# Kernel optimization log

Hardware: AMD Instinct MI355X
Metric: run time of the kernel (lower is better)

The kernel has to match this reference:

```python
import jax, jax.numpy as jnp
import numpy as np

IN_F, OUT_F = 512, 512
GRID_SIZE, SPLINE_ORDER = 5, 3
K = GRID_SIZE + SPLINE_ORDER  # 8 basis functions
B, S = 8, 1024


def setup_inputs() -> dict:
    key = jax.random.key(0)
    k1, k2, k3, k4, k5 = jax.random.split(key, 5)
    return {
        "x": jax.random.normal(k1, (B, S, IN_F), dtype=jnp.float32),
        "coeff": jax.random.normal(k2, (OUT_F, IN_F, K), dtype=jnp.float32),
        "scale_base": jax.random.normal(k3, (OUT_F, IN_F), dtype=jnp.float32) * 0.1,
        "scale_spline": jax.random.normal(k4, (OUT_F, IN_F), dtype=jnp.float32),
        "base_bias": jax.random.normal(k5, (OUT_F, IN_F), dtype=jnp.float32),
    }


def reference(x, coeff, scale_base, scale_spline, base_bias):
    batch = x.shape[0]
    in_f = x.shape[-1]
    k = coeff.shape[-1]

    xc = jnp.clip(x.reshape(-1, in_f), -1.0, 1.0)      # (N, in)
    base = jax.nn.silu(xc)                              # (N, in)

    # polynomial basis recurrence: b0 = 1, b1 = x, b_i = 2*x*b_{i-1} - 1
    bases = [jnp.ones_like(xc), xc]
    for _ in range(2, k):
        bases.append(2.0 * xc * bases[-1] - 1.0)
    basis = jnp.stack(bases[:k], axis=-1)               # (N, in, K)

    # spline[n,o] = sum_{i,k} scale_spline[o,i]*coeff[o,i,k]*basis[n,i,k]
    w_spline = scale_spline[..., None] * coeff          # (out, in, K)
    spline_term = jnp.einsum('nik,oik->no', basis, w_spline)
    base_term = base @ scale_base.T                     # (N, out)
    out = base_term + spline_term + jnp.sum(base_bias, axis=1)  # (N, out)

    out = out.reshape(batch, -1, base_bias.shape[0])    # (B, S, out)
    if out.shape[-2] == 1:
        out = out[..., 0, :]
    return out
```

## Files before the change

### kernel.cpp

```cpp
#include <hip/hip_runtime.h>
#include <hip/hip_bf16.h>

#define IN_FEAT 512
#define OUT_FEAT 512
#define NTOK 8192
#define KDIM 4096

#define BM 128
#define BN 64
#define BK 64
#define LDA 72
#define LDB 72

typedef short bf16x8 __attribute__((ext_vector_type(8)));
typedef float f32x4 __attribute__((ext_vector_type(4)));

static __device__ inline short f2bf(float f) {
    union { float f; unsigned u; } v; v.f = f;
    unsigned u = v.u;
    u += 0x7fffu + ((u >> 16) & 1u);
    return (short)(u >> 16);
}

__global__ __launch_bounds__(256) void kan_prep(
    const float* __restrict__ coeff, const float* __restrict__ scale_base,
    const float* __restrict__ scale_spline, const float* __restrict__ base_bias,
    short* __restrict__ Wb, float* __restrict__ bias)
{
    int o = blockIdx.x;
    int tid = threadIdx.x;
    float local = 0.f;
#pragma unroll
    for (int rep = 0; rep < 2; ++rep) {
        int i = tid + rep * 256;
        size_t oi = (size_t)o * IN_FEAT + i;
        const float4* c4 = (const float4*)(coeff + oi * 8);
        float4 ca = c4[0], cb = c4[1];
        float ss = scale_spline[oi];
        float sb = scale_base[oi];
        local += base_bias[oi] + ss * ca.x;
        bf16x8 w;
        w[0] = f2bf(sb);
        w[1] = f2bf(ss * ca.y); w[2] = f2bf(ss * ca.z); w[3] = f2bf(ss * ca.w);
        w[4] = f2bf(ss * cb.x); w[5] = f2bf(ss * cb.y); w[6] = f2bf(ss * cb.z);
        w[7] = f2bf(ss * cb.w);
        *(bf16x8*)(Wb + (size_t)o * KDIM + (size_t)i * 8) = w;
    }
    __shared__ float red[4];
    for (int off = 32; off > 0; off >>= 1) local += __shfl_down(local, off, 64);
    int lane = tid & 63, wv = tid >> 6;
    if (lane == 0) red[wv] = local;
    __syncthreads();
    if (tid == 0) bias[o] = red[0] + red[1] + red[2] + red[3];
}

__global__ __launch_bounds__(256) void kan_gemm(
    const float* __restrict__ x, const short* __restrict__ Wb,
    const float* __restrict__ bias, float* __restrict__ out)
{
    __shared__ __align__(16) short As[BM * LDA];
    __shared__ __align__(16) short Bs[BN * LDB];

    int tid = threadIdx.x;
    int mb = blockIdx.x >> 3;
    int nb = blockIdx.x & 7;
    int m0 = mb * BM, o0 = nb * BN;

    int lane = tid & 63, wv = tid >> 6;
    int wm = wv >> 1, wn = wv & 1;
    int qd = lane >> 4, ln15 = lane & 15;

    f32x4 acc[4][2];
#pragma unroll
    for (int a = 0; a < 4; ++a)
#pragma unroll
        for (int b = 0; b < 2; ++b) acc[a][b] = (f32x4)0.f;

    int n_local = tid >> 1;
    int half = tid & 1;
    const float4* xrow = (const float4*)(x + (size_t)(m0 + n_local) * IN_FEAT);

    for (int it = 0; it < IN_FEAT / 8; ++it) {
        float4 xv = xrow[it * 2 + half];
        float xs[4] = {xv.x, xv.y, xv.z, xv.w};
#pragma unroll
        for (int ii = 0; ii < 4; ++ii) {
            float xc = fminf(fmaxf(xs[ii], -1.f), 1.f);
            float base = xc / (1.f + __expf(-xc));
            bf16x8 fr;
            fr[0] = f2bf(base);
            float t = xc;
            fr[1] = f2bf(t);
#pragma unroll
            for (int f = 2; f < 8; ++f) { t = 2.f * xc * t - 1.f; fr[f] = f2bf(t); }
            *(bf16x8*)&As[n_local * LDA + half * 32 + ii * 8] = fr;
        }
#pragma unroll
        for (int rep = 0; rep < 2; ++rep) {
            int c = tid + rep * 256;
            int row = c >> 3, cc = c & 7;
            bf16x8 wfrag = *(const bf16x8*)(Wb + (size_t)(o0 + row) * KDIM + it * BK + cc * 8);
            *(bf16x8*)&Bs[row * LDB + cc * 8] = wfrag;
        }
        __syncthreads();
#pragma unroll
        for (int kq = 0; kq < 2; ++kq) {
            bf16x8 af[4], bfr[2];
#pragma unroll
            for (int fm = 0; fm < 4; ++fm)
                af[fm] = *(const bf16x8*)&As[(wm * 64 + fm * 16 + ln15) * LDA + kq * 32 + qd * 8];
#pragma unroll
            for (int fn = 0; fn < 2; ++fn)
                bfr[fn] = *(const bf16x8*)&Bs[(wn * 32 + fn * 16 + ln15) * LDB + kq * 32 + qd * 8];
#pragma unroll
            for (int fm = 0; fm < 4; ++fm)
#pragma unroll
                for (int fn = 0; fn < 2; ++fn)
                    acc[fm][fn] = __builtin_amdgcn_mfma_f32_16x16x32_bf16(
                        af[fm], bfr[fn], acc[fm][fn], 0, 0, 0);
        }
        __syncthreads();
    }

#pragma unroll
    for (int fn = 0; fn < 2; ++fn) {
        int o = o0 + wn * 32 + fn * 16 + ln15;
        float bv = bias[o];
#pragma unroll
        for (int fm = 0; fm < 4; ++fm) {
            int r0 = m0 + wm * 64 + fm * 16 + qd * 4;
#pragma unroll
            for (int r = 0; r < 4; ++r)
                out[(size_t)(r0 + r) * OUT_FEAT + o] = acc[fm][fn][r] + bv;
        }
    }
}

extern "C" void kernel_launch(void* const* d_in, const int* in_sizes, int n_in,
                              void* d_out, int out_size, void* d_ws, size_t ws_size,
                              hipStream_t stream) {
    const float* x            = (const float*)d_in[0];
    const float* coeff        = (const float*)d_in[1];
    const float* scale_base   = (const float*)d_in[2];
    const float* scale_spline = (const float*)d_in[3];
    const float* base_bias    = (const float*)d_in[4];
    float* out = (float*)d_out;

    short* Wb   = (short*)d_ws;
    float* bias = (float*)((char*)d_ws + (size_t)OUT_FEAT * KDIM * 2);

    kan_prep<<<OUT_FEAT, 256, 0, stream>>>(coeff, scale_base, scale_spline, base_bias, Wb, bias);
    kan_gemm<<<(NTOK / BM) * (OUT_FEAT / BN), 256, 0, stream>>>(x, Wb, bias, out);
}
```

Before: 156.9 us.

## Materialize bf16 basis matrix and use split-K direct-to-LDS GEMM with atomics

Adds a separate kernel that expands x into the full bf16 basis matrix A (N×4096) in workspace, so the GEMM no longer recomputes the basis per output tile. The new GEMM uses 128×128 tiles, async global_load_lds transfers into XOR-swizzled LDS, and a split-K of 2 whose partials are accumulated with float atomics into an output pre-filled with the bias. This removes redundant basis computation and register-staged loads. In exchange it writes and reads a 64MB intermediate and adds atomic traffic. The old fused path is kept as a fallback when the workspace is too small.

```diff
diff --git a/kernel.cpp b/kernel.cpp
--- a/kernel.cpp
+++ b/kernel.cpp
@@ -5,12 +5,6 @@
 #define OUT_FEAT 512
 #define NTOK 8192
 #define KDIM 4096
-
-#define BM 128
-#define BN 64
-#define BK 64
-#define LDA 72
-#define LDB 72
 
 typedef short bf16x8 __attribute__((ext_vector_type(8)));
 typedef float f32x4 __attribute__((ext_vector_type(4)));
@@ -20,6 +14,13 @@
     unsigned u = v.u;
     u += 0x7fffu + ((u >> 16) & 1u);
     return (short)(u >> 16);
+}
+
+static __device__ inline void gload_lds16(const short* g, short* l) {
+    __builtin_amdgcn_global_load_lds(
+        (const __attribute__((address_space(1))) unsigned int*)g,
+        (__attribute__((address_space(3))) unsigned int*)l,
+        16, 0, 0);
 }
 
 __global__ __launch_bounds__(256) void kan_prep(
@@ -54,12 +55,121 @@
     if (tid == 0) bias[o] = red[0] + red[1] + red[2] + red[3];
 }
 
-__global__ __launch_bounds__(256) void kan_gemm(
+__global__ __launch_bounds__(256) void kan_agen(
+    const float* __restrict__ x, short* __restrict__ A)
+{
+    int idx = blockIdx.x * 256 + threadIdx.x;
+    float xv = x[idx];
+    float xc = fminf(fmaxf(xv, -1.f), 1.f);
+    float base = xc / (1.f + __expf(-xc));
+    bf16x8 fr;
+    fr[0] = f2bf(base);
+    float t = xc;
+    fr[1] = f2bf(t);
+#pragma unroll
+    for (int f = 2; f < 8; ++f) { t = 2.f * xc * t - 1.f; fr[f] = f2bf(t); }
+    *(bf16x8*)(A + (size_t)idx * 8) = fr;
+}
+
+__global__ __launch_bounds__(256) void kan_init_out(
+    const float* __restrict__ bias, float* __restrict__ out)
+{
+    int idx = blockIdx.x * 256 + threadIdx.x;
+    int o4 = idx & (OUT_FEAT / 4 - 1);
+    ((float4*)out)[idx] = ((const float4*)bias)[o4];
+}
+
+#define GBM 128
+#define GBN 128
+#define GBK 64
+
+__global__ __launch_bounds__(256) void kan_gemm2(
+    const short* __restrict__ A, const short* __restrict__ Wb,
+    float* __restrict__ out)
+{
+    __shared__ __align__(16) short As[GBM * GBK];
+    __shared__ __align__(16) short Bs[GBN * GBK];
+
+    int tid = threadIdx.x;
+    int nb = blockIdx.x, mb = blockIdx.y, ks = blockIdx.z;
+    int m0 = mb * GBM, o0 = nb * GBN, k0 = ks * (KDIM / 2);
+
+    int lane = tid & 63, wv = tid >> 6;
+    int wm = wv >> 1, wn = wv & 1;
+    int qd = lane >> 4, ln15 = lane & 15;
+
+    f32x4 acc[4][4];
+#pragma unroll
+    for (int a = 0; a < 4; ++a)
+#pragma unroll
+        for (int b = 0; b < 4; ++b) acc[a][b] = (f32x4)0.f;
+
+    int rg = lane >> 3;
+    int c_log = (lane & 7) ^ rg;
+    const short* Ag = A  + (size_t)(m0 + wv * 32 + rg) * KDIM + k0 + c_log * 8;
+    const short* Bg = Wb + (size_t)(o0 + wv * 32 + rg) * KDIM + k0 + c_log * 8;
+
+    for (int it = 0; it < (KDIM / 2) / GBK; ++it) {
+        const short* a_it = Ag + it * GBK;
+        const short* b_it = Bg + it * GBK;
+#pragma unroll
+        for (int j = 0; j < 4; ++j)
+            gload_lds16(a_it + (size_t)j * 8 * KDIM, &As[(wv * 32 + j * 8) * GBK]);
+#pragma unroll
+        for (int j = 0; j < 4; ++j)
+            gload_lds16(b_it + (size_t)j * 8 * KDIM, &Bs[(wv * 32 + j * 8) * GBK]);
+        __syncthreads();
+
+#pragma unroll
+        for (int kq = 0; kq < 2; ++kq) {
+            bf16x8 af[4], bf[4];
+#pragma unroll
+            for (int fm = 0; fm < 4; ++fm) {
+                int row = wm * 64 + fm * 16 + ln15;
+                int p = (kq * 4 + qd) ^ (row & 7);
+                af[fm] = *(const bf16x8*)&As[row * GBK + p * 8];
+            }
+#pragma unroll
+            for (int fn = 0; fn < 4; ++fn) {
+                int row = wn * 64 + fn * 16 + ln15;
+                int p = (kq * 4 + qd) ^ (row & 7);
+                bf[fn] = *(const bf16x8*)&Bs[row * GBK + p * 8];
+            }
+#pragma unroll
+            for (int fm = 0; fm < 4; ++fm)
+#pragma unroll
+                for (int fn = 0; fn < 4; ++fn)
+                    acc[fm][fn] = __builtin_amdgcn_mfma_f32_16x16x32_bf16(
+                        af[fm], bf[fn], acc[fm][fn], 0, 0, 0);
+        }
+        __syncthreads();
+    }
+
+#pragma unroll
+    for (int fn = 0; fn < 4; ++fn) {
+        int o = o0 + wn * 64 + fn * 16 + ln15;
+#pragma unroll
+        for (int fm = 0; fm < 4; ++fm) {
+            int r0 = m0 + wm * 64 + fm * 16 + qd * 4;
+#pragma unroll
+            for (int r = 0; r < 4; ++r)
+                atomicAdd(&out[(size_t)(r0 + r) * OUT_FEAT + o], acc[fm][fn][r]);
+        }
+    }
+}
+
+#define BM 128
+#define BN 64
+#define BK 64
+#define LDA 72
+#define LDB 72
+
+__global__ __launch_bounds__(256) void kan_gemm_fused(
     const float* __restrict__ x, const short* __restrict__ Wb,
     const float* __restrict__ bias, float* __restrict__ out)
 {
-    __shared__ __align__(16) short As[BM * LDA];
-    __shared__ __align__(16) short Bs[BN * LDB];
+    __shared__ __align__(16) short Asf[BM * LDA];
+    __shared__ __align__(16) short Bsf[BN * LDB];
 
     int tid = threadIdx.x;
     int mb = blockIdx.x >> 3;
@@ -93,14 +203,14 @@
             fr[1] = f2bf(t);
 #pragma unroll
             for (int f = 2; f < 8; ++f) { t = 2.f * xc * t - 1.f; fr[f] = f2bf(t); }
-            *(bf16x8*)&As[n_local * LDA + half * 32 + ii * 8] = fr;
+            *(bf16x8*)&Asf[n_local * LDA + half * 32 + ii * 8] = fr;
         }
 #pragma unroll
         for (int rep = 0; rep < 2; ++rep) {
             int c = tid + rep * 256;
             int row = c >> 3, cc = c & 7;
             bf16x8 wfrag = *(const bf16x8*)(Wb + (size_t)(o0 + row) * KDIM + it * BK + cc * 8);
-            *(bf16x8*)&Bs[row * LDB + cc * 8] = wfrag;
+            *(bf16x8*)&Bsf[row * LDB + cc * 8] = wfrag;
         }
         __syncthreads();
 #pragma unroll
@@ -108,10 +218,10 @@
             bf16x8 af[4], bfr[2];
 #pragma unroll
             for (int fm = 0; fm < 4; ++fm)
-                af[fm] = *(const bf16x8*)&As[(wm * 64 + fm * 16 + ln15) * LDA + kq * 32 + qd * 8];
+                af[fm] = *(const bf16x8*)&Asf[(wm * 64 + fm * 16 + ln15) * LDA + kq * 32 + qd * 8];
 #pragma unroll
             for (int fn = 0; fn < 2; ++fn)
-                bfr[fn] = *(const bf16x8*)&Bs[(wn * 32 + fn * 16 + ln15) * LDB + kq * 32 + qd * 8];
+                bfr[fn] = *(const bf16x8*)&Bsf[(wn * 32 + fn * 16 + ln15) * LDB + kq * 32 + qd * 8];
 #pragma unroll
             for (int fm = 0; fm < 4; ++fm)
 #pragma unroll
@@ -146,9 +256,22 @@
     const float* base_bias    = (const float*)d_in[4];
     float* out = (float*)d_out;
 
+    const size_t WB_BYTES   = (size_t)OUT_FEAT * KDIM * 2;
+    const size_t BIAS_OFF   = WB_BYTES;
+    const size_t A_OFF      = WB_BYTES + 65536;
+    const size_t A_BYTES    = (size_t)NTOK * KDIM * 2;
     short* Wb   = (short*)d_ws;
-    float* bias = (float*)((char*)d_ws + (size_t)OUT_FEAT * KDIM * 2);
+    float* bias = (float*)((char*)d_ws + BIAS_OFF);
 
     kan_prep<<<OUT_FEAT, 256, 0, stream>>>(coeff, scale_base, scale_spline, base_bias, Wb, bias);
-    kan_gemm<<<(NTOK / BM) * (OUT_FEAT / BN), 256, 0, stream>>>(x, Wb, bias, out);
-}
+
+    if (ws_size >= A_OFF + A_BYTES) {
+        short* A = (short*)((char*)d_ws + A_OFF);
+        kan_agen<<<NTOK * IN_FEAT / 256, 256, 0, stream>>>(x, A);
+        kan_init_out<<<NTOK * OUT_FEAT / 4 / 256, 256, 0, stream>>>(bias, out);
+        dim3 grid(OUT_FEAT / GBN, NTOK / GBM, 2);
+        kan_gemm2<<<grid, 256, 0, stream>>>(A, Wb, out);
+    } else {
+        kan_gemm_fused<<<(NTOK / BM) * (OUT_FEAT / BN), 256, 0, stream>>>(x, Wb, bias, out);
+    }
+}
```

Measured after the change: 160.6 us. 2.4% more time.

## Double-buffer GEMM tiles with direct global-to-LDS weight loads and XOR swizzle

Applied to the files above, without the earlier changes.

Rewrites the fused basis+GEMM kernel to double-buffer the A and B shared-memory tiles, so the next K-slice's basis generation and weight fetch overlap the current MFMA work and only one barrier is needed per iteration. Weight tiles are loaded straight into LDS with global_load_lds instead of passing through registers, and an XOR swizzle replaces padding to avoid bank conflicts. The tile shape changes from 128x64 to 64x128, and bf16 packing now uses a perm-based round (add 0x8000) instead of round-to-nearest-even. Risks include slightly different rounding, more LDS per block, and a different x recompute ratio: each token's basis is now built by 4 column blocks rather than 8.

```diff
diff --git a/kernel.cpp b/kernel.cpp
--- a/kernel.cpp
+++ b/kernel.cpp
@@ -6,11 +6,9 @@
 #define NTOK 8192
 #define KDIM 4096
 
-#define BM 128
-#define BN 64
+#define BM 64
+#define BN 128
 #define BK 64
-#define LDA 72
-#define LDB 72
 
 typedef short bf16x8 __attribute__((ext_vector_type(8)));
 typedef float f32x4 __attribute__((ext_vector_type(4)));
@@ -20,6 +18,18 @@
     unsigned u = v.u;
     u += 0x7fffu + ((u >> 16) & 1u);
     return (short)(u >> 16);
+}
+
+static __device__ inline unsigned pack2bf(float f0, float f1) {
+    union { float f; unsigned u; } a, b; a.f = f0; b.f = f1;
+    return __builtin_amdgcn_perm(b.u + 0x8000u, a.u + 0x8000u, 0x07060302u);
+}
+
+static __device__ inline void gload_lds16(const short* g, short* l) {
+    __builtin_amdgcn_global_load_lds(
+        (const __attribute__((address_space(1))) unsigned int*)g,
+        (__attribute__((address_space(3))) unsigned int*)l,
+        16, 0, 0);
 }
 
 __global__ __launch_bounds__(256) void kan_prep(
@@ -54,86 +64,109 @@
     if (tid == 0) bias[o] = red[0] + red[1] + red[2] + red[3];
 }
 
-__global__ __launch_bounds__(256) void kan_gemm(
+__global__ __launch_bounds__(256) void kan_gemm3(
     const float* __restrict__ x, const short* __restrict__ Wb,
     const float* __restrict__ bias, float* __restrict__ out)
 {
-    __shared__ __align__(16) short As[BM * LDA];
-    __shared__ __align__(16) short Bs[BN * LDB];
+    __shared__ __align__(16) short As[2][BM * BK];
+    __shared__ __align__(16) short Bs[2][BN * BK];
 
     int tid = threadIdx.x;
-    int mb = blockIdx.x >> 3;
-    int nb = blockIdx.x & 7;
+    int nb = blockIdx.x & 3;
+    int mb = blockIdx.x >> 2;
     int m0 = mb * BM, o0 = nb * BN;
 
     int lane = tid & 63, wv = tid >> 6;
-    int wm = wv >> 1, wn = wv & 1;
+    int wm = wv & 1, wn = wv >> 1;
     int qd = lane >> 4, ln15 = lane & 15;
 
-    f32x4 acc[4][2];
+    f32x4 acc[2][4];
 #pragma unroll
-    for (int a = 0; a < 4; ++a)
+    for (int a = 0; a < 2; ++a)
 #pragma unroll
-        for (int b = 0; b < 2; ++b) acc[a][b] = (f32x4)0.f;
+        for (int b = 0; b < 4; ++b) acc[a][b] = (f32x4)0.f;
 
-    int n_local = tid >> 1;
-    int half = tid & 1;
-    const float4* xrow = (const float4*)(x + (size_t)(m0 + n_local) * IN_FEAT);
+    int tok = tid >> 2;
+    int c0  = (tid & 3) * 2;
+    const float2* xp = (const float2*)(x + (size_t)(m0 + tok) * IN_FEAT) + (tid & 3);
 
-    for (int it = 0; it < IN_FEAT / 8; ++it) {
-        float4 xv = xrow[it * 2 + half];
-        float xs[4] = {xv.x, xv.y, xv.z, xv.w};
+    int rg = lane >> 3;
+    int c_log = (lane & 7) ^ rg;
+    const short* Bg = Wb + (size_t)(o0 + wv * 32 + rg) * KDIM + c_log * 8;
+
+#define GEN_CHUNK(xval, cc, buf)                                              \
+    {                                                                         \
+        float xc = fminf(fmaxf((xval), -1.f), 1.f);                           \
+        float bse = xc / (1.f + __expf(-xc));                                 \
+        float b2 = 2.f * xc * xc - 1.f;                                       \
+        float b3 = 2.f * xc * b2 - 1.f;                                       \
+        float b4 = 2.f * xc * b3 - 1.f;                                       \
+        float b5 = 2.f * xc * b4 - 1.f;                                       \
+        float b6 = 2.f * xc * b5 - 1.f;                                       \
+        float b7 = 2.f * xc * b6 - 1.f;                                       \
+        uint4 pk;                                                             \
+        pk.x = pack2bf(bse, xc); pk.y = pack2bf(b2, b3);                      \
+        pk.z = pack2bf(b4, b5);  pk.w = pack2bf(b6, b7);                      \
+        *(uint4*)&As[buf][tok * BK + ((cc) ^ (tok & 7)) * 8] = pk;            \
+    }
+
+    {
+        float2 xv = xp[0];
+        GEN_CHUNK(xv.x, c0, 0);
+        GEN_CHUNK(xv.y, c0 + 1, 0);
 #pragma unroll
-        for (int ii = 0; ii < 4; ++ii) {
-            float xc = fminf(fmaxf(xs[ii], -1.f), 1.f);
-            float base = xc / (1.f + __expf(-xc));
-            bf16x8 fr;
-            fr[0] = f2bf(base);
-            float t = xc;
-            fr[1] = f2bf(t);
+        for (int j = 0; j < 4; ++j)
+            gload_lds16(Bg + (size_t)j * 8 * KDIM, &Bs[0][(wv * 32 + j * 8) * BK]);
+    }
+
+    int cur = 0;
+    for (int it = 0; it < IN_FEAT / 8; ++it, cur ^= 1) {
+        __syncthreads();
+        if (it < IN_FEAT / 8 - 1) {
+            int nxt = cur ^ 1;
 #pragma unroll
-            for (int f = 2; f < 8; ++f) { t = 2.f * xc * t - 1.f; fr[f] = f2bf(t); }
-            *(bf16x8*)&As[n_local * LDA + half * 32 + ii * 8] = fr;
+            for (int j = 0; j < 4; ++j)
+                gload_lds16(Bg + (it + 1) * BK + (size_t)j * 8 * KDIM,
+                            &Bs[nxt][(wv * 32 + j * 8) * BK]);
+            float2 xv = xp[(it + 1) * 4];
+            GEN_CHUNK(xv.x, c0, nxt);
+            GEN_CHUNK(xv.y, c0 + 1, nxt);
         }
 #pragma unroll
-        for (int rep = 0; rep < 2; ++rep) {
-            int c = tid + rep * 256;
-            int row = c >> 3, cc = c & 7;
-            bf16x8 wfrag = *(const bf16x8*)(Wb + (size_t)(o0 + row) * KDIM + it * BK + cc * 8);
-            *(bf16x8*)&Bs[row * LDB + cc * 8] = wfrag;
+        for (int kq = 0; kq < 2; ++kq) {
+            bf16x8 af[2], bf[4];
+#pragma unroll
+            for (int fm = 0; fm < 2; ++fm) {
+                int row = wm * 32 + fm * 16 + ln15;
+                af[fm] = *(const bf16x8*)&As[cur][row * BK + ((kq * 4 + qd) ^ (row & 7)) * 8];
+            }
+#pragma unroll
+            for (int fn = 0; fn < 4; ++fn) {
+                int row = wn * 64 + fn * 16 + ln15;
+                bf[fn] = *(const bf16x8*)&Bs[cur][row * BK + ((kq * 4 + qd) ^ (row & 7)) * 8];
+            }
+#pragma unroll
+            for (int fm = 0; fm < 2; ++fm)
+#pragma unroll
+                for (int fn = 0; fn < 4; ++fn)
+                    acc[fm][fn] = __builtin_amdgcn_mfma_f32_16x16x32_bf16(
+                        af[fm], bf[fn], acc[fm][fn], 0, 0, 0);
         }
-        __syncthreads();
-#pragma unroll
-        for (int kq = 0; kq < 2; ++kq) {
-            bf16x8 af[4], bfr[2];
-#pragma unroll
-            for (int fm = 0; fm < 4; ++fm)
-                af[fm] = *(const bf16x8*)&As[(wm * 64 + fm * 16 + ln15) * LDA + kq * 32 + qd * 8];
-#pragma unroll
-            for (int fn = 0; fn < 2; ++fn)
-                bfr[fn] = *(const bf16x8*)&Bs[(wn * 32 + fn * 16 + ln15) * LDB + kq * 32 + qd * 8];
-#pragma unroll
-            for (int fm = 0; fm < 4; ++fm)
-#pragma unroll
-                for (int fn = 0; fn < 2; ++fn)
-                    acc[fm][fn] = __builtin_amdgcn_mfma_f32_16x16x32_bf16(
-                        af[fm], bfr[fn], acc[fm][fn], 0, 0, 0);
-        }
-        __syncthreads();
     }
 
 #pragma unroll
-    for (int fn = 0; fn < 2; ++fn) {
-        int o = o0 + wn * 32 + fn * 16 + ln15;
+    for (int fn = 0; fn < 4; ++fn) {
+        int o = o0 + wn * 64 + fn * 16 + ln15;
         float bv = bias[o];
 #pragma unroll
-        for (int fm = 0; fm < 4; ++fm) {
-            int r0 = m0 + wm * 64 + fm * 16 + qd * 4;
+        for (int fm = 0; fm < 2; ++fm) {
+            int r0 = m0 + wm * 32 + fm * 16 + qd * 4;
 #pragma unroll
             for (int r = 0; r < 4; ++r)
                 out[(size_t)(r0 + r) * OUT_FEAT + o] = acc[fm][fn][r] + bv;
         }
     }
+#undef GEN_CHUNK
 }
 
 extern "C" void kernel_launch(void* const* d_in, const int* in_sizes, int n_in,
@@ -150,5 +183,5 @@
     float* bias = (float*)((char*)d_ws + (size_t)OUT_FEAT * KDIM * 2);
 
     kan_prep<<<OUT_FEAT, 256, 0, stream>>>(coeff, scale_base, scale_spline, base_bias, Wb, bias);
-    kan_gemm<<<(NTOK / BM) * (OUT_FEAT / BN), 256, 0, stream>>>(x, Wb, bias, out);
+    kan_gemm3<<<(NTOK / BM) * (OUT_FEAT / BN), 256, 0, stream>>>(x, Wb, bias, out);
 }
```

Result: faster. 145.4 us (-7.3%).

## Drop LDS staging; feed MFMA fragments straight from registers with prefetch

Applied to the files above, without the earlier changes.

The GEMM kernel now skips shared memory. Each lane loads its own x values and weight fragments from global memory straight into registers, computes the basis expansion in registers, and prefetches the next K-slice while the current one runs. The output tile grows to 128x128 per block, with a 4x4 MFMA fragment grid per wave, and both barriers are gone. In exchange, each wave recomputes the basis for its rows and global loads become narrow, scattered per-lane reads. Register pressure also rises, which is why launch bounds now allow only one block.

```diff
diff --git a/kernel.cpp b/kernel.cpp
--- a/kernel.cpp
+++ b/kernel.cpp
@@ -5,12 +5,6 @@
 #define OUT_FEAT 512
 #define NTOK 8192
 #define KDIM 4096
-
-#define BM 128
-#define BN 64
-#define BK 64
-#define LDA 72
-#define LDB 72
 
 typedef short bf16x8 __attribute__((ext_vector_type(8)));
 typedef float f32x4 __attribute__((ext_vector_type(4)));
@@ -20,6 +14,29 @@
     unsigned u = v.u;
     u += 0x7fffu + ((u >> 16) & 1u);
     return (short)(u >> 16);
+}
+
+static __device__ inline unsigned pack2bf(float f0, float f1) {
+    union { float f; unsigned u; } a, b; a.f = f0; b.f = f1;
+    return __builtin_amdgcn_perm(b.u + 0x8000u, a.u + 0x8000u, 0x07060302u);
+}
+
+static __device__ inline bf16x8 gen_chunk(float xv) {
+    float xc = fminf(fmaxf(xv, -1.f), 1.f);
+    float e  = __expf(-xc);
+    float bse = xc * __builtin_amdgcn_rcpf(1.f + e);
+    float b2 = 2.f * xc * xc - 1.f;
+    float b3 = 2.f * xc * b2 - 1.f;
+    float b4 = 2.f * xc * b3 - 1.f;
+    float b5 = 2.f * xc * b4 - 1.f;
+    float b6 = 2.f * xc * b5 - 1.f;
+    float b7 = 2.f * xc * b6 - 1.f;
+    union { uint4 u; bf16x8 v; } r;
+    r.u.x = pack2bf(bse, xc);
+    r.u.y = pack2bf(b2, b3);
+    r.u.z = pack2bf(b4, b5);
+    r.u.w = pack2bf(b6, b7);
+    return r.v;
 }
 
 __global__ __launch_bounds__(256) void kan_prep(
@@ -54,77 +71,83 @@
     if (tid == 0) bias[o] = red[0] + red[1] + red[2] + red[3];
 }
 
-__global__ __launch_bounds__(256) void kan_gemm(
+__global__ __launch_bounds__(256, 1) void kan_gemm5(
     const float* __restrict__ x, const short* __restrict__ Wb,
     const float* __restrict__ bias, float* __restrict__ out)
 {
-    __shared__ __align__(16) short As[BM * LDA];
-    __shared__ __align__(16) short Bs[BN * LDB];
-
     int tid = threadIdx.x;
-    int mb = blockIdx.x >> 3;
-    int nb = blockIdx.x & 7;
-    int m0 = mb * BM, o0 = nb * BN;
+    int nb = blockIdx.x & 3;
+    int mb = blockIdx.x >> 2;
+    int m0 = mb * 128, o0 = nb * 128;
 
     int lane = tid & 63, wv = tid >> 6;
-    int wm = wv >> 1, wn = wv & 1;
+    int wm = wv & 1, wn = wv >> 1;
     int qd = lane >> 4, ln15 = lane & 15;
 
-    f32x4 acc[4][2];
+    f32x4 acc[4][4];
 #pragma unroll
     for (int a = 0; a < 4; ++a)
 #pragma unroll
-        for (int b = 0; b < 2; ++b) acc[a][b] = (f32x4)0.f;
+        for (int b = 0; b < 4; ++b) acc[a][b] = (f32x4)0.f;
 
-    int n_local = tid >> 1;
-    int half = tid & 1;
-    const float4* xrow = (const float4*)(x + (size_t)(m0 + n_local) * IN_FEAT);
+    const float* xb[4];
+#pragma unroll
+    for (int fm = 0; fm < 4; ++fm)
+        xb[fm] = x + (size_t)(m0 + wm * 64 + fm * 16 + ln15) * IN_FEAT + qd;
+    const short* wr[4];
+#pragma unroll
+    for (int fn = 0; fn < 4; ++fn)
+        wr[fn] = Wb + (size_t)(o0 + wn * 64 + fn * 16 + ln15) * KDIM + qd * 8;
 
+    float  xc_[8];
+    bf16x8 bc_[8];
+#pragma unroll
+    for (int fm = 0; fm < 4; ++fm)
+#pragma unroll
+        for (int kq = 0; kq < 2; ++kq)
+            xc_[fm * 2 + kq] = xb[fm][kq * 4];
+#pragma unroll
+    for (int fn = 0; fn < 4; ++fn)
+#pragma unroll
+        for (int kq = 0; kq < 2; ++kq)
+            bc_[fn * 2 + kq] = *(const bf16x8*)(wr[fn] + kq * 32);
+
+#pragma unroll 2
     for (int it = 0; it < IN_FEAT / 8; ++it) {
-        float4 xv = xrow[it * 2 + half];
-        float xs[4] = {xv.x, xv.y, xv.z, xv.w};
+        int itn = (it + 1) & 63;
+        float  xn_[8];
+        bf16x8 bn_[8];
 #pragma unroll
-        for (int ii = 0; ii < 4; ++ii) {
-            float xc = fminf(fmaxf(xs[ii], -1.f), 1.f);
-            float base = xc / (1.f + __expf(-xc));
-            bf16x8 fr;
-            fr[0] = f2bf(base);
-            float t = xc;
-            fr[1] = f2bf(t);
+        for (int fm = 0; fm < 4; ++fm)
 #pragma unroll
-            for (int f = 2; f < 8; ++f) { t = 2.f * xc * t - 1.f; fr[f] = f2bf(t); }
-            *(bf16x8*)&As[n_local * LDA + half * 32 + ii * 8] = fr;
-        }
+            for (int kq = 0; kq < 2; ++kq)
+                xn_[fm * 2 + kq] = xb[fm][itn * 8 + kq * 4];
 #pragma unroll
-        for (int rep = 0; rep < 2; ++rep) {
-            int c = tid + rep * 256;
-            int row = c >> 3, cc = c & 7;
-            bf16x8 wfrag = *(const bf16x8*)(Wb + (size_t)(o0 + row) * KDIM + it * BK + cc * 8);
-            *(bf16x8*)&Bs[row * LDB + cc * 8] = wfrag;
-        }
-        __syncthreads();
+        for (int fn = 0; fn < 4; ++fn)
+#pragma unroll
+            for (int kq = 0; kq < 2; ++kq)
+                bn_[fn * 2 + kq] = *(const bf16x8*)(wr[fn] + itn * 64 + kq * 32);
+
 #pragma unroll
         for (int kq = 0; kq < 2; ++kq) {
-            bf16x8 af[4], bfr[2];
+            bf16x8 af[4];
 #pragma unroll
             for (int fm = 0; fm < 4; ++fm)
-                af[fm] = *(const bf16x8*)&As[(wm * 64 + fm * 16 + ln15) * LDA + kq * 32 + qd * 8];
-#pragma unroll
-            for (int fn = 0; fn < 2; ++fn)
-                bfr[fn] = *(const bf16x8*)&Bs[(wn * 32 + fn * 16 + ln15) * LDB + kq * 32 + qd * 8];
+                af[fm] = gen_chunk(xc_[fm * 2 + kq]);
 #pragma unroll
             for (int fm = 0; fm < 4; ++fm)
 #pragma unroll
-                for (int fn = 0; fn < 2; ++fn)
+                for (int fn = 0; fn < 4; ++fn)
                     acc[fm][fn] = __builtin_amdgcn_mfma_f32_16x16x32_bf16(
-                        af[fm], bfr[fn], acc[fm][fn], 0, 0, 0);
+                        af[fm], bc_[fn * 2 + kq], acc[fm][fn], 0, 0, 0);
         }
-        __syncthreads();
+#pragma unroll
+        for (int i = 0; i < 8; ++i) { xc_[i] = xn_[i]; bc_[i] = bn_[i]; }
     }
 
 #pragma unroll
-    for (int fn = 0; fn < 2; ++fn) {
-        int o = o0 + wn * 32 + fn * 16 + ln15;
+    for (int fn = 0; fn < 4; ++fn) {
+        int o = o0 + wn * 64 + fn * 16 + ln15;
         float bv = bias[o];
 #pragma unroll
         for (int fm = 0; fm < 4; ++fm) {
@@ -150,5 +173,5 @@
     float* bias = (float*)((char*)d_ws + (size_t)OUT_FEAT * KDIM * 2);
 
     kan_prep<<<OUT_FEAT, 256, 0, stream>>>(coeff, scale_base, scale_spline, base_bias, Wb, bias);
-    kan_gemm<<<(NTOK / BM) * (OUT_FEAT / BN), 256, 0, stream>>>(x, Wb, bias, out);
+    kan_gemm5<<<(NTOK / 128) * (OUT_FEAT / 128), 256, 0, stream>>>(x, Wb, bias, out);
 }
```

New measurement: 193.4 us. 23.2% more time.
